# Optimization experiments

Measured on AMD Instinct MI355X. Metric: run time of the kernel, lower is better.

## Reference

```python
import jax, jax.numpy as jnp
import numpy as np

N_NODES = 50000
N_EDGES = 800000
FEAT = 128
HID = 64
N_CLS = 12


def setup_inputs() -> dict:
    key = jax.random.key(0)
    ks = jax.random.split(key, 8)
    x = jax.random.normal(ks[0], (N_NODES, FEAT), dtype=jnp.float32)
    edge_index = jax.random.randint(ks[1], (2, N_EDGES), 0, N_NODES, dtype=jnp.int64)
    s1 = 1.0 / np.sqrt(FEAT)
    s2 = 1.0 / np.sqrt(HID)
    W1 = jax.random.uniform(ks[2], (FEAT, HID), jnp.float32, -s1, s1)
    b1 = jnp.zeros((HID,), jnp.float32)
    W2 = jax.random.uniform(ks[3], (HID, HID), jnp.float32, -s2, s2)
    b2 = jnp.zeros((HID,), jnp.float32)
    Wfc = jax.random.uniform(ks[4], (HID, N_CLS), jnp.float32, -s2, s2)
    bfc = jax.random.uniform(ks[5], (N_CLS,), jnp.float32, -s2, s2)
    return {"x": x, "edge_index": edge_index, "W1": W1, "b1": b1,
            "W2": W2, "b2": b2, "Wfc": Wfc, "bfc": bfc}


def gcn_conv(x, W, b, src, dst, n_nodes):
    """PyG GCNConv: symmetric-normalized aggregation with self-loops.
    out_i = sum_{j in N(i)} (xW)_j / sqrt(d_i d_j) + (xW)_i / d_i + b,
    where d = in-degree + 1 (self loop)."""
    xw = x @ W  # [N, out] -- transform before propagate (PyG order)
    deg = jnp.zeros((n_nodes,), x.dtype).at[dst].add(1.0) + 1.0
    dinv = jax.lax.rsqrt(deg)
    norm = dinv[src] * dinv[dst]  # [E]
    agg = jax.ops.segment_sum(xw[src] * norm[:, None], dst, num_segments=n_nodes)
    agg = agg + xw * (dinv * dinv)[:, None]  # self-loop term
    return agg + b


def reference(x, edge_index, W1, b1, W2, b2, Wfc, bfc):
    n = x.shape[0]
    src, dst = edge_index[0], edge_index[1]
    h = jax.nn.relu(gcn_conv(x, W1, b1, src, dst, n))
    h = jax.nn.relu(gcn_conv(h, W2, b2, src, dst, n))
    return h @ Wfc + bfc  # [N, num_content_categories]
```

## Files before the change

### kernel.cpp

```cpp
#include <hip/hip_runtime.h>
#include <hip/hip_fp16.h>


#define CAP   64
#define NBUK  196
#define ET    2048
#define NB    391

typedef unsigned short u16;

__global__ __launch_bounds__(256) void k_hist(const int* __restrict__ dst,
                                              int* __restrict__ blkcnt, int E) {
    __shared__ int hist[NBUK];
    const int tid = threadIdx.x, blk = blockIdx.x;
    for (int i = tid; i < NBUK; i += 256) hist[i] = 0;
    __syncthreads();
    const int e0 = blk * ET;
#pragma unroll
    for (int j = 0; j < ET / 256; j++) {
        int e = e0 + j * 256 + tid;
        if (e < E) atomicAdd(&hist[(unsigned)dst[e] >> 8], 1);
    }
    __syncthreads();
    for (int b = tid; b < NBUK; b += 256) blkcnt[b * NB + blk] = hist[b];
}

__global__ __launch_bounds__(512) void k_scanA(int* __restrict__ blkcnt,
                                               int* __restrict__ btot) {
    __shared__ int s[512];
    const int t = threadIdx.x, b = blockIdx.x;
    int v = (t < NB) ? blkcnt[b * NB + t] : 0;
    s[t] = v;
    __syncthreads();
#pragma unroll
    for (int d = 1; d < 512; d <<= 1) {
        int u = (t >= d) ? s[t - d] : 0;
        __syncthreads();
        s[t] += u;
        __syncthreads();
    }
    if (t < NB) blkcnt[b * NB + t] = s[t] - v;
    if (t == 511) btot[b] = s[511];
}

__global__ __launch_bounds__(256) void k_scanB(const int* __restrict__ btot,
                                               int* __restrict__ bbase, int E) {
    __shared__ int s[256];
    const int t = threadIdx.x;
    int v = (t < NBUK) ? btot[t] : 0;
    s[t] = v;
    __syncthreads();
#pragma unroll
    for (int d = 1; d < 256; d <<= 1) {
        int u = (t >= d) ? s[t - d] : 0;
        __syncthreads();
        s[t] += u;
        __syncthreads();
    }
    if (t < NBUK) bbase[t] = s[t] - v;
    if (t == 0) bbase[NBUK] = E;
}

__global__ __launch_bounds__(256) void k_scatter(const int* __restrict__ src,
                                                 const int* __restrict__ dst,
                                                 const int* __restrict__ blkcnt,
                                                 const int* __restrict__ bbase,
                                                 unsigned* __restrict__ eb, int E) {
    __shared__ int cur[NBUK];
    const int tid = threadIdx.x, blk = blockIdx.x;
    for (int i = tid; i < NBUK; i += 256) cur[i] = blkcnt[i * NB + blk] + bbase[i];
    __syncthreads();
    const int e0 = blk * ET;
#pragma unroll
    for (int j = 0; j < ET / 256; j++) {
        int e = e0 + j * 256 + tid;
        if (e < E) {
            unsigned d = (unsigned)dst[e];
            unsigned u = (d << 16) | (unsigned)src[e];
            int p = atomicAdd(&cur[d >> 8], 1);
            eb[p] = u;
        }
    }
}

__global__ __launch_bounds__(1024) void k_buildb(const unsigned* __restrict__ eb,
                                                 const int* __restrict__ bbase,
                                                 u16* __restrict__ csr,
                                                 int* __restrict__ cnt, int n) {
    __shared__ u16 lcsr[256 * CAP];
    __shared__ int cur[256];
    const int tid = threadIdx.x, b = blockIdx.x;
    if (tid < 256) cur[tid] = 0;
    __syncthreads();
    const int e0 = bbase[b], e1 = bbase[b + 1];
    for (int e = e0 + tid; e < e1; e += 1024) {
        unsigned u = eb[e];
        int ld = (int)((u >> 16) & 255u);
        int p = atomicAdd(&cur[ld], 1);
        if (p < CAP) lcsr[ld * CAP + p] = (u16)(u & 0xffffu);
    }
    __syncthreads();
    const int node0 = b * 256;
    for (int i = tid; i < 256 * CAP / 8; i += 1024) {
        int r = i / (CAP / 8), q = i % (CAP / 8);
        int c = cur[r] < CAP ? cur[r] : CAP;
        uint4 v = *(uint4*)&lcsr[r * CAP + q * 8];
        if (q * 8 >= c) v = make_uint4(0, 0, 0, 0);
        *(uint4*)&csr[(size_t)(node0 + r) * CAP + q * 8] = v;
    }
    if (tid < 256 && node0 + tid < n) cnt[node0 + tid] = cur[tid];
}

template <int K, bool IS_HALF, typename TIN>
__global__ __launch_bounds__(256) void k_gemm(const TIN* __restrict__ X,
                                              const float* __restrict__ W,
                                              const int* __restrict__ cnt,
                                              __half* __restrict__ Y, int n) {
    constexpr int KC = 64;
    constexpr int XS = KC + 4;
    __shared__ float ws[KC * 64];
    __shared__ float xs[64 * XS];
    const int tid = threadIdx.x;
    const int tx = tid & 15;
    const int ty = tid >> 4;
    const int row0 = blockIdx.x * 64;

    float acc[4][4];
#pragma unroll
    for (int r = 0; r < 4; r++)
#pragma unroll
        for (int c = 0; c < 4; c++) acc[r][c] = 0.f;

#pragma unroll 1
    for (int kc = 0; kc < K; kc += KC) {
        for (int i = tid; i < KC * 16; i += 256) {
            int kk = i >> 4, c4 = i & 15;
            *(float4*)&ws[kk * 64 + 4 * c4] = *(const float4*)&W[(kc + kk) * 64 + 4 * c4];
        }
        if (IS_HALF) {
            for (int i = tid; i < 64 * (KC / 8); i += 256) {
                int r = i >> 3, q = i & 7;
                uint4 u = make_uint4(0, 0, 0, 0);
                int row = row0 + r;
                if (row < n) u = *(const uint4*)&X[(size_t)row * K + kc + 8 * q];
                float2 f0 = __half22float2(*(__half2*)&u.x);
                float2 f1 = __half22float2(*(__half2*)&u.y);
                float2 f2 = __half22float2(*(__half2*)&u.z);
                float2 f3 = __half22float2(*(__half2*)&u.w);
                *(float4*)&xs[r * XS + 8 * q]     = make_float4(f0.x, f0.y, f1.x, f1.y);
                *(float4*)&xs[r * XS + 8 * q + 4] = make_float4(f2.x, f2.y, f3.x, f3.y);
            }
        } else {
            for (int i = tid; i < 64 * (KC / 4); i += 256) {
                int r = i / (KC / 4), q = i % (KC / 4);
                float4 v = make_float4(0.f, 0.f, 0.f, 0.f);
                int row = row0 + r;
                if (row < n) v = *(const float4*)&((const float*)X)[(size_t)row * K + kc + 4 * q];
                *(float4*)&xs[r * XS + 4 * q] = v;
            }
        }
        __syncthreads();

#pragma unroll 2
        for (int q = 0; q < KC / 4; q++) {
            float4 xv[4];
#pragma unroll
            for (int r = 0; r < 4; r++)
                xv[r] = *(const float4*)&xs[(ty + 16 * r) * XS + 4 * q];
#pragma unroll
            for (int kk = 0; kk < 4; kk++) {
                float4 wv = *(const float4*)&ws[(4 * q + kk) * 64 + 4 * tx];
#pragma unroll
                for (int r = 0; r < 4; r++) {
                    float xval = (kk == 0) ? xv[r].x : (kk == 1) ? xv[r].y
                               : (kk == 2) ? xv[r].z : xv[r].w;
                    acc[r][0] = fmaf(xval, wv.x, acc[r][0]);
                    acc[r][1] = fmaf(xval, wv.y, acc[r][1]);
                    acc[r][2] = fmaf(xval, wv.z, acc[r][2]);
                    acc[r][3] = fmaf(xval, wv.w, acc[r][3]);
                }
            }
        }
        __syncthreads();
    }

#pragma unroll
    for (int r = 0; r < 4; r++) {
        int row = row0 + ty + 16 * r;
        if (row < n) {
            float d = rsqrtf((float)cnt[row] + 1.0f);
            __half2* yh = (__half2*)&Y[(size_t)row * 64 + 4 * tx];
            yh[0] = __floats2half2_rn(acc[r][0] * d, acc[r][1] * d);
            yh[1] = __floats2half2_rn(acc[r][2] * d, acc[r][3] * d);
        }
    }
}

__device__ __forceinline__ float2 gather_node(const __half* __restrict__ y,
                                              const u16* __restrict__ lst,
                                              int deg, int c2) {
    float2 acc = make_float2(0.f, 0.f);
    int i = 0;
    for (; i + 16 <= deg; i += 16) {
        uint4 qa = *(const uint4*)(lst + i);
        uint4 qb = *(const uint4*)(lst + i + 8);
        unsigned idx[16] = {qa.x & 0xffffu, qa.x >> 16, qa.y & 0xffffu, qa.y >> 16,
                            qa.z & 0xffffu, qa.z >> 16, qa.w & 0xffffu, qa.w >> 16,
                            qb.x & 0xffffu, qb.x >> 16, qb.y & 0xffffu, qb.y >> 16,
                            qb.z & 0xffffu, qb.z >> 16, qb.w & 0xffffu, qb.w >> 16};
        __half2 v[16];
#pragma unroll
        for (int t = 0; t < 16; t++) v[t] = *(const __half2*)&y[idx[t] * 64 + 2 * c2];
        float2 f[16];
#pragma unroll
        for (int t = 0; t < 16; t++) f[t] = __half22float2(v[t]);
#pragma unroll
        for (int s = 1; s < 16; s <<= 1)
#pragma unroll
            for (int t = 0; t < 16; t += 2 * s) { f[t].x += f[t + s].x; f[t].y += f[t + s].y; }
        acc.x += f[0].x; acc.y += f[0].y;
    }
    if (i + 8 <= deg) {
        uint4 qa = *(const uint4*)(lst + i);
        unsigned idx[8] = {qa.x & 0xffffu, qa.x >> 16, qa.y & 0xffffu, qa.y >> 16,
                           qa.z & 0xffffu, qa.z >> 16, qa.w & 0xffffu, qa.w >> 16};
        __half2 v[8];
#pragma unroll
        for (int t = 0; t < 8; t++) v[t] = *(const __half2*)&y[idx[t] * 64 + 2 * c2];
        float2 f[8];
#pragma unroll
        for (int t = 0; t < 8; t++) f[t] = __half22float2(v[t]);
#pragma unroll
        for (int s = 1; s < 8; s <<= 1)
#pragma unroll
            for (int t = 0; t < 8; t += 2 * s) { f[t].x += f[t + s].x; f[t].y += f[t + s].y; }
        acc.x += f[0].x; acc.y += f[0].y;
        i += 8;
    }
    if (i + 4 <= deg) {
        uint2 qa = *(const uint2*)(lst + i);
        unsigned idx[4] = {qa.x & 0xffffu, qa.x >> 16, qa.y & 0xffffu, qa.y >> 16};
        __half2 v[4];
#pragma unroll
        for (int t = 0; t < 4; t++) v[t] = *(const __half2*)&y[idx[t] * 64 + 2 * c2];
        float2 f0 = __half22float2(v[0]), f1 = __half22float2(v[1]);
        float2 f2 = __half22float2(v[2]), f3 = __half22float2(v[3]);
        acc.x += (f0.x + f1.x) + (f2.x + f3.x);
        acc.y += (f0.y + f1.y) + (f2.y + f3.y);
        i += 4;
    }
    for (; i < deg; i++) {
        float2 f = __half22float2(*(const __half2*)&y[lst[i] * 64 + 2 * c2]);
        acc.x += f.x; acc.y += f.y;
    }
    return acc;
}

__global__ __launch_bounds__(256) void k_agg1(const __half* __restrict__ y,
                                              const u16* __restrict__ csr,
                                              const int* __restrict__ cnt,
                                              const float* __restrict__ bias,
                                              __half* __restrict__ h1, int n) {
    const int tid = threadIdx.x;
    const int c2 = tid & 31;
    const int node = blockIdx.x * 8 + (tid >> 5);
    if (node >= n) return;
    int deg_raw = cnt[node];
    int deg = deg_raw > CAP ? CAP : deg_raw;
    float2 acc = gather_node(y, csr + node * CAP, deg, c2);
    float2 sf = __half22float2(*(const __half2*)&y[node * 64 + 2 * c2]);
    float d = rsqrtf((float)deg_raw + 1.0f);
    float2 bv = *(const float2*)&bias[2 * c2];
    float vx = fmaxf(fmaf(d, acc.x + sf.x, bv.x), 0.f);
    float vy = fmaxf(fmaf(d, acc.y + sf.y, bv.y), 0.f);
    *(__half2*)&h1[node * 64 + 2 * c2] = __floats2half2_rn(vx, vy);
}

__global__ __launch_bounds__(256) void k_agg2fc(const __half* __restrict__ y,
                                                const u16* __restrict__ csr,
                                                const int* __restrict__ cnt,
                                                const float* __restrict__ bias,
                                                const float* __restrict__ Wfc,
                                                const float* __restrict__ bfc,
                                                float* __restrict__ out, int n) {
    __shared__ float wf[12 * 64];
    __shared__ float bf[12];
    const int tid = threadIdx.x;
    for (int i = tid; i < 12 * 64; i += 256) {
        int c = i >> 6, k = i & 63;
        wf[i] = Wfc[k * 12 + c];
    }
    if (tid < 12) bf[tid] = bfc[tid];
    __syncthreads();

    const int c2 = tid & 31;
    const int node = blockIdx.x * 8 + (tid >> 5);
    if (node >= n) return;
    int deg_raw = cnt[node];
    int deg = deg_raw > CAP ? CAP : deg_raw;
    float2 acc = gather_node(y, csr + node * CAP, deg, c2);
    float2 sf = __half22float2(*(const __half2*)&y[node * 64 + 2 * c2]);
    float d = rsqrtf((float)deg_raw + 1.0f);
    float2 bv = *(const float2*)&bias[2 * c2];
    float vx = fmaxf(fmaf(d, acc.x + sf.x, bv.x), 0.f);
    float vy = fmaxf(fmaf(d, acc.y + sf.y, bv.y), 0.f);

    float res = 0.f;
#pragma unroll
    for (int c = 0; c < 12; c++) {
        float2 wv = *(const float2*)&wf[c * 64 + 2 * c2];
        float p = vx * wv.x + vy * wv.y;
        p += __shfl_xor(p, 1);
        p += __shfl_xor(p, 2);
        p += __shfl_xor(p, 4);
        p += __shfl_xor(p, 8);
        p += __shfl_xor(p, 16);
        if (c2 == c) res = p + bf[c];
    }
    if (c2 < 12) out[(size_t)node * 12 + c2] = res;
}

extern "C" void kernel_launch(void* const* d_in, const int* in_sizes, int n_in,
                              void* d_out, int out_size, void* d_ws, size_t ws_size,
                              hipStream_t stream) {
    const float* x   = (const float*)d_in[0];
    const int*   ei  = (const int*)d_in[1];
    const float* W1  = (const float*)d_in[2];
    const float* b1  = (const float*)d_in[3];
    const float* W2  = (const float*)d_in[4];
    const float* b2  = (const float*)d_in[5];
    const float* Wfc = (const float*)d_in[6];
    const float* bfc = (const float*)d_in[7];
    float* out = (float*)d_out;

    const int n = in_sizes[0] / 128;
    const int E = in_sizes[1] / 2;
    const int* src = ei;
    const int* dst = ei + E;

    char* w = (char*)d_ws;
    unsigned* eb  = (unsigned*)w;  w += (size_t)((E + 63) / 64) * 64 * 4;
    int* blkcnt   = (int*)w;       w += (size_t)NBUK * NB * 4 + 256;
    int* btot     = (int*)w;       w += 256 * 4;
    int* bbase    = (int*)w;       w += (NBUK + 64) * 4;
    int* cnt      = (int*)w;       w += (size_t)((n + 63) / 64) * 64 * 4;
    u16* csr      = (u16*)w;       w += (size_t)NBUK * 256 * CAP * 2;
    __half* y     = (__half*)w;    w += (size_t)n * 64 * 2;
    __half* h1    = (__half*)w;

    k_hist   <<<dim3(NB), dim3(256), 0, stream>>>(dst, blkcnt, E);
    k_scanA  <<<dim3(NBUK), dim3(512), 0, stream>>>(blkcnt, btot);
    k_scanB  <<<dim3(1), dim3(256), 0, stream>>>(btot, bbase, E);
    k_scatter<<<dim3(NB), dim3(256), 0, stream>>>(src, dst, blkcnt, bbase, eb, E);
    k_buildb <<<dim3(NBUK), dim3(1024), 0, stream>>>(eb, bbase, csr, cnt, n);
    k_gemm<128, false, float><<<dim3((n + 63) / 64), dim3(256), 0, stream>>>(x, W1, cnt, y, n);
    k_agg1   <<<dim3((n + 7) / 8), dim3(256), 0, stream>>>(y, csr, cnt, b1, h1, n);
    k_gemm<64, true, __half><<<dim3((n + 63) / 64), dim3(256), 0, stream>>>(h1, W2, cnt, y, n);
    k_agg2fc <<<dim3((n + 7) / 8), dim3(256), 0, stream>>>(y, csr, cnt, b2, Wfc, bfc, out, n);
}
```

Baseline: 189.6 us.

## Vectorize edge loads, fold bucket scan into consumers, widen gather to 4 channels

Doubles edges per block in the histogram and scatter kernels and loads src/dst as int4 vectors. The separate single-block bucket scan kernel is removed; each scatter and buildb block recomputes the 196-entry prefix in shared memory instead. The aggregation kernels now have 16 lanes per node, each gathering 4 half channels per neighbor with uint2 loads, which halves the load instruction count and shortens the FC shuffle reduction. The trade-offs are redundant per-block scan work and fewer blocks for the preprocessing stages.

```diff
diff --git a/kernel.cpp b/kernel.cpp
--- a/kernel.cpp
+++ b/kernel.cpp
@@ -4,8 +4,8 @@
 
 #define CAP   64
 #define NBUK  196
-#define ET    2048
-#define NB    391
+#define ET    4096
+#define NB    196
 
 typedef unsigned short u16;
 
@@ -16,83 +16,112 @@
     for (int i = tid; i < NBUK; i += 256) hist[i] = 0;
     __syncthreads();
     const int e0 = blk * ET;
-#pragma unroll
-    for (int j = 0; j < ET / 256; j++) {
-        int e = e0 + j * 256 + tid;
-        if (e < E) atomicAdd(&hist[(unsigned)dst[e] >> 8], 1);
+    if (e0 + ET <= E) {
+        const int4* d4 = (const int4*)(dst + e0);
+#pragma unroll
+        for (int j = 0; j < ET / 1024; j++) {
+            int4 d = d4[j * 256 + tid];
+            atomicAdd(&hist[(unsigned)d.x >> 8], 1);
+            atomicAdd(&hist[(unsigned)d.y >> 8], 1);
+            atomicAdd(&hist[(unsigned)d.z >> 8], 1);
+            atomicAdd(&hist[(unsigned)d.w >> 8], 1);
+        }
+    } else {
+        for (int j = 0; j < ET / 256; j++) {
+            int e = e0 + j * 256 + tid;
+            if (e < E) atomicAdd(&hist[(unsigned)dst[e] >> 8], 1);
+        }
     }
     __syncthreads();
     for (int b = tid; b < NBUK; b += 256) blkcnt[b * NB + blk] = hist[b];
 }
 
-__global__ __launch_bounds__(512) void k_scanA(int* __restrict__ blkcnt,
+__global__ __launch_bounds__(256) void k_scanA(int* __restrict__ blkcnt,
                                                int* __restrict__ btot) {
-    __shared__ int s[512];
+    __shared__ int s[256];
     const int t = threadIdx.x, b = blockIdx.x;
     int v = (t < NB) ? blkcnt[b * NB + t] : 0;
     s[t] = v;
     __syncthreads();
 #pragma unroll
-    for (int d = 1; d < 512; d <<= 1) {
-        int u = (t >= d) ? s[t - d] : 0;
-        __syncthreads();
-        s[t] += u;
-        __syncthreads();
-    }
-    if (t < NB) blkcnt[b * NB + t] = s[t] - v;
-    if (t == 511) btot[b] = s[511];
-}
-
-__global__ __launch_bounds__(256) void k_scanB(const int* __restrict__ btot,
-                                               int* __restrict__ bbase, int E) {
-    __shared__ int s[256];
-    const int t = threadIdx.x;
-    int v = (t < NBUK) ? btot[t] : 0;
-    s[t] = v;
-    __syncthreads();
-#pragma unroll
     for (int d = 1; d < 256; d <<= 1) {
         int u = (t >= d) ? s[t - d] : 0;
         __syncthreads();
         s[t] += u;
         __syncthreads();
     }
-    if (t < NBUK) bbase[t] = s[t] - v;
-    if (t == 0) bbase[NBUK] = E;
+    if (t < NB) blkcnt[b * NB + t] = s[t] - v;
+    if (t == 255) btot[b] = s[255];
+}
+
+__device__ __forceinline__ void local_bucket_scan(const int* __restrict__ btot,
+                                                  int* bb, int tid) {
+    if (tid < 256) bb[tid] = (tid < NBUK) ? btot[tid] : 0;
+    __syncthreads();
+#pragma unroll
+    for (int d = 1; d < 256; d <<= 1) {
+        int u = 0;
+        if (tid < 256 && tid >= d) u = bb[tid - d];
+        __syncthreads();
+        if (tid < 256) bb[tid] += u;
+        __syncthreads();
+    }
+    if (tid < 256) bb[tid] -= (tid < NBUK) ? btot[tid] : 0;
+    __syncthreads();
 }
 
 __global__ __launch_bounds__(256) void k_scatter(const int* __restrict__ src,
                                                  const int* __restrict__ dst,
                                                  const int* __restrict__ blkcnt,
-                                                 const int* __restrict__ bbase,
+                                                 const int* __restrict__ btot,
                                                  unsigned* __restrict__ eb, int E) {
+    __shared__ int bb[256];
     __shared__ int cur[NBUK];
     const int tid = threadIdx.x, blk = blockIdx.x;
-    for (int i = tid; i < NBUK; i += 256) cur[i] = blkcnt[i * NB + blk] + bbase[i];
+    local_bucket_scan(btot, bb, tid);
+    for (int i = tid; i < NBUK; i += 256) cur[i] = blkcnt[i * NB + blk] + bb[i];
     __syncthreads();
     const int e0 = blk * ET;
-#pragma unroll
-    for (int j = 0; j < ET / 256; j++) {
-        int e = e0 + j * 256 + tid;
-        if (e < E) {
-            unsigned d = (unsigned)dst[e];
-            unsigned u = (d << 16) | (unsigned)src[e];
-            int p = atomicAdd(&cur[d >> 8], 1);
-            eb[p] = u;
+    if (e0 + ET <= E) {
+        const int4* s4 = (const int4*)(src + e0);
+        const int4* d4 = (const int4*)(dst + e0);
+#pragma unroll
+        for (int j = 0; j < ET / 1024; j++) {
+            int4 sv = s4[j * 256 + tid];
+            int4 dv = d4[j * 256 + tid];
+            unsigned u0 = ((unsigned)dv.x << 16) | (unsigned)sv.x;
+            unsigned u1 = ((unsigned)dv.y << 16) | (unsigned)sv.y;
+            unsigned u2 = ((unsigned)dv.z << 16) | (unsigned)sv.z;
+            unsigned u3 = ((unsigned)dv.w << 16) | (unsigned)sv.w;
+            eb[atomicAdd(&cur[u0 >> 24], 1)] = u0;
+            eb[atomicAdd(&cur[u1 >> 24], 1)] = u1;
+            eb[atomicAdd(&cur[u2 >> 24], 1)] = u2;
+            eb[atomicAdd(&cur[u3 >> 24], 1)] = u3;
+        }
+    } else {
+        for (int j = 0; j < ET / 256; j++) {
+            int e = e0 + j * 256 + tid;
+            if (e < E) {
+                unsigned d = (unsigned)dst[e];
+                unsigned u = (d << 16) | (unsigned)src[e];
+                eb[atomicAdd(&cur[d >> 8], 1)] = u;
+            }
         }
     }
 }
 
 __global__ __launch_bounds__(1024) void k_buildb(const unsigned* __restrict__ eb,
-                                                 const int* __restrict__ bbase,
+                                                 const int* __restrict__ btot,
                                                  u16* __restrict__ csr,
                                                  int* __restrict__ cnt, int n) {
+    __shared__ int bb[256];
     __shared__ u16 lcsr[256 * CAP];
     __shared__ int cur[256];
     const int tid = threadIdx.x, b = blockIdx.x;
+    local_bucket_scan(btot, bb, tid);
     if (tid < 256) cur[tid] = 0;
     __syncthreads();
-    const int e0 = bbase[b], e1 = bbase[b + 1];
+    const int e0 = bb[b], e1 = bb[b] + btot[b];
     for (int e = e0 + tid; e < e1; e += 1024) {
         unsigned u = eb[e];
         int ld = (int)((u >> 16) & 255u);
@@ -196,10 +225,11 @@
     }
 }
 
-__device__ __forceinline__ float2 gather_node(const __half* __restrict__ y,
+__device__ __forceinline__ float4 gather_node(const __half* __restrict__ y,
                                               const u16* __restrict__ lst,
-                                              int deg, int c2) {
-    float2 acc = make_float2(0.f, 0.f);
+                                              int deg, int c4) {
+    float4 a0 = make_float4(0.f, 0.f, 0.f, 0.f);
+    float4 a1 = make_float4(0.f, 0.f, 0.f, 0.f);
     int i = 0;
     for (; i + 16 <= deg; i += 16) {
         uint4 qa = *(const uint4*)(lst + i);
@@ -208,52 +238,61 @@
                             qa.z & 0xffffu, qa.z >> 16, qa.w & 0xffffu, qa.w >> 16,
                             qb.x & 0xffffu, qb.x >> 16, qb.y & 0xffffu, qb.y >> 16,
                             qb.z & 0xffffu, qb.z >> 16, qb.w & 0xffffu, qb.w >> 16};
-        __half2 v[16];
-#pragma unroll
-        for (int t = 0; t < 16; t++) v[t] = *(const __half2*)&y[idx[t] * 64 + 2 * c2];
-        float2 f[16];
-#pragma unroll
-        for (int t = 0; t < 16; t++) f[t] = __half22float2(v[t]);
-#pragma unroll
-        for (int s = 1; s < 16; s <<= 1)
-#pragma unroll
-            for (int t = 0; t < 16; t += 2 * s) { f[t].x += f[t + s].x; f[t].y += f[t + s].y; }
-        acc.x += f[0].x; acc.y += f[0].y;
+        uint2 v[16];
+#pragma unroll
+        for (int t = 0; t < 16; t++) v[t] = *(const uint2*)&y[idx[t] * 64 + 4 * c4];
+#pragma unroll
+        for (int t = 0; t < 16; t += 2) {
+            float2 lo0 = __half22float2(*(__half2*)&v[t].x);
+            float2 hi0 = __half22float2(*(__half2*)&v[t].y);
+            float2 lo1 = __half22float2(*(__half2*)&v[t + 1].x);
+            float2 hi1 = __half22float2(*(__half2*)&v[t + 1].y);
+            a0.x += lo0.x; a0.y += lo0.y; a0.z += hi0.x; a0.w += hi0.y;
+            a1.x += lo1.x; a1.y += lo1.y; a1.z += hi1.x; a1.w += hi1.y;
+        }
     }
     if (i + 8 <= deg) {
         uint4 qa = *(const uint4*)(lst + i);
         unsigned idx[8] = {qa.x & 0xffffu, qa.x >> 16, qa.y & 0xffffu, qa.y >> 16,
                            qa.z & 0xffffu, qa.z >> 16, qa.w & 0xffffu, qa.w >> 16};
-        __half2 v[8];
-#pragma unroll
-        for (int t = 0; t < 8; t++) v[t] = *(const __half2*)&y[idx[t] * 64 + 2 * c2];
-        float2 f[8];
-#pragma unroll
-        for (int t = 0; t < 8; t++) f[t] = __half22float2(v[t]);
-#pragma unroll
-        for (int s = 1; s < 8; s <<= 1)
-#pragma unroll
-            for (int t = 0; t < 8; t += 2 * s) { f[t].x += f[t + s].x; f[t].y += f[t + s].y; }
-        acc.x += f[0].x; acc.y += f[0].y;
+        uint2 v[8];
+#pragma unroll
+        for (int t = 0; t < 8; t++) v[t] = *(const uint2*)&y[idx[t] * 64 + 4 * c4];
+#pragma unroll
+        for (int t = 0; t < 8; t += 2) {
+            float2 lo0 = __half22float2(*(__half2*)&v[t].x);
+            float2 hi0 = __half22float2(*(__half2*)&v[t].y);
+            float2 lo1 = __half22float2(*(__half2*)&v[t + 1].x);
+            float2 hi1 = __half22float2(*(__half2*)&v[t + 1].y);
+            a0.x += lo0.x; a0.y += lo0.y; a0.z += hi0.x; a0.w += hi0.y;
+            a1.x += lo1.x; a1.y += lo1.y; a1.z += hi1.x; a1.w += hi1.y;
+        }
         i += 8;
     }
     if (i + 4 <= deg) {
         uint2 qa = *(const uint2*)(lst + i);
         unsigned idx[4] = {qa.x & 0xffffu, qa.x >> 16, qa.y & 0xffffu, qa.y >> 16};
-        __half2 v[4];
-#pragma unroll
-        for (int t = 0; t < 4; t++) v[t] = *(const __half2*)&y[idx[t] * 64 + 2 * c2];
-        float2 f0 = __half22float2(v[0]), f1 = __half22float2(v[1]);
-        float2 f2 = __half22float2(v[2]), f3 = __half22float2(v[3]);
-        acc.x += (f0.x + f1.x) + (f2.x + f3.x);
-        acc.y += (f0.y + f1.y) + (f2.y + f3.y);
+        uint2 v[4];
+#pragma unroll
+        for (int t = 0; t < 4; t++) v[t] = *(const uint2*)&y[idx[t] * 64 + 4 * c4];
+#pragma unroll
+        for (int t = 0; t < 4; t += 2) {
+            float2 lo0 = __half22float2(*(__half2*)&v[t].x);
+            float2 hi0 = __half22float2(*(__half2*)&v[t].y);
+            float2 lo1 = __half22float2(*(__half2*)&v[t + 1].x);
+            float2 hi1 = __half22float2(*(__half2*)&v[t + 1].y);
+            a0.x += lo0.x; a0.y += lo0.y; a0.z += hi0.x; a0.w += hi0.y;
+            a1.x += lo1.x; a1.y += lo1.y; a1.z += hi1.x; a1.w += hi1.y;
+        }
         i += 4;
     }
     for (; i < deg; i++) {
-        float2 f = __half22float2(*(const __half2*)&y[lst[i] * 64 + 2 * c2]);
-        acc.x += f.x; acc.y += f.y;
-    }
-    return acc;
+        uint2 vv = *(const uint2*)&y[lst[i] * 64 + 4 * c4];
+        float2 lo = __half22float2(*(__half2*)&vv.x);
+        float2 hi = __half22float2(*(__half2*)&vv.y);
+        a0.x += lo.x; a0.y += lo.y; a0.z += hi.x; a0.w += hi.y;
+    }
+    return make_float4(a0.x + a1.x, a0.y + a1.y, a0.z + a1.z, a0.w + a1.w);
 }
 
 __global__ __launch_bounds__(256) void k_agg1(const __half* __restrict__ y,
@@ -262,18 +301,25 @@
                                               const float* __restrict__ bias,
                                               __half* __restrict__ h1, int n) {
     const int tid = threadIdx.x;
-    const int c2 = tid & 31;
-    const int node = blockIdx.x * 8 + (tid >> 5);
+    const int c4 = tid & 15;
+    const int node = blockIdx.x * 16 + (tid >> 4);
     if (node >= n) return;
     int deg_raw = cnt[node];
     int deg = deg_raw > CAP ? CAP : deg_raw;
-    float2 acc = gather_node(y, csr + node * CAP, deg, c2);
-    float2 sf = __half22float2(*(const __half2*)&y[node * 64 + 2 * c2]);
+    float4 acc = gather_node(y, csr + node * CAP, deg, c4);
+    uint2 sv = *(const uint2*)&y[node * 64 + 4 * c4];
+    float2 slo = __half22float2(*(__half2*)&sv.x);
+    float2 shi = __half22float2(*(__half2*)&sv.y);
     float d = rsqrtf((float)deg_raw + 1.0f);
-    float2 bv = *(const float2*)&bias[2 * c2];
-    float vx = fmaxf(fmaf(d, acc.x + sf.x, bv.x), 0.f);
-    float vy = fmaxf(fmaf(d, acc.y + sf.y, bv.y), 0.f);
-    *(__half2*)&h1[node * 64 + 2 * c2] = __floats2half2_rn(vx, vy);
+    float4 bv = *(const float4*)&bias[4 * c4];
+    float v0 = fmaxf(fmaf(d, acc.x + slo.x, bv.x), 0.f);
+    float v1 = fmaxf(fmaf(d, acc.y + slo.y, bv.y), 0.f);
+    float v2 = fmaxf(fmaf(d, acc.z + shi.x, bv.z), 0.f);
+    float v3 = fmaxf(fmaf(d, acc.w + shi.y, bv.w), 0.f);
+    uint2 o;
+    *(__half2*)&o.x = __floats2half2_rn(v0, v1);
+    *(__half2*)&o.y = __floats2half2_rn(v2, v3);
+    *(uint2*)&h1[node * 64 + 4 * c4] = o;
 }
 
 __global__ __launch_bounds__(256) void k_agg2fc(const __half* __restrict__ y,
@@ -293,31 +339,34 @@
     if (tid < 12) bf[tid] = bfc[tid];
     __syncthreads();
 
-    const int c2 = tid & 31;
-    const int node = blockIdx.x * 8 + (tid >> 5);
+    const int c4 = tid & 15;
+    const int node = blockIdx.x * 16 + (tid >> 4);
     if (node >= n) return;
     int deg_raw = cnt[node];
     int deg = deg_raw > CAP ? CAP : deg_raw;
-    float2 acc = gather_node(y, csr + node * CAP, deg, c2);
-    float2 sf = __half22float2(*(const __half2*)&y[node * 64 + 2 * c2]);
+    float4 acc = gather_node(y, csr + node * CAP, deg, c4);
+    uint2 sv = *(const uint2*)&y[node * 64 + 4 * c4];
+    float2 slo = __half22float2(*(__half2*)&sv.x);
+    float2 shi = __half22float2(*(__half2*)&sv.y);
     float d = rsqrtf((float)deg_raw + 1.0f);
-    float2 bv = *(const float2*)&bias[2 * c2];
-    float vx = fmaxf(fmaf(d, acc.x + sf.x, bv.x), 0.f);
-    float vy = fmaxf(fmaf(d, acc.y + sf.y, bv.y), 0.f);
+    float4 bv = *(const float4*)&bias[4 * c4];
+    float v0 = fmaxf(fmaf(d, acc.x + slo.x, bv.x), 0.f);
+    float v1 = fmaxf(fmaf(d, acc.y + slo.y, bv.y), 0.f);
+    float v2 = fmaxf(fmaf(d, acc.z + shi.x, bv.z), 0.f);
+    float v3 = fmaxf(fmaf(d, acc.w + shi.y, bv.w), 0.f);
 
     float res = 0.f;
 #pragma unroll
     for (int c = 0; c < 12; c++) {
-        float2 wv = *(const float2*)&wf[c * 64 + 2 * c2];
-        float p = vx * wv.x + vy * wv.y;
+        float4 wv = *(const float4*)&wf[c * 64 + 4 * c4];
+        float p = v0 * wv.x + v1 * wv.y + v2 * wv.z + v3 * wv.w;
         p += __shfl_xor(p, 1);
         p += __shfl_xor(p, 2);
         p += __shfl_xor(p, 4);
         p += __shfl_xor(p, 8);
-        p += __shfl_xor(p, 16);
-        if (c2 == c) res = p + bf[c];
-    }
-    if (c2 < 12) out[(size_t)node * 12 + c2] = res;
+        if (c4 == c) res = p + bf[c];
+    }
+    if (c4 < 12) out[(size_t)node * 12 + c4] = res;
 }
 
 extern "C" void kernel_launch(void* const* d_in, const int* in_sizes, int n_in,
@@ -337,24 +386,23 @@
     const int E = in_sizes[1] / 2;
     const int* src = ei;
     const int* dst = ei + E;
+    const int nblk = (E + ET - 1) / ET;
 
     char* w = (char*)d_ws;
     unsigned* eb  = (unsigned*)w;  w += (size_t)((E + 63) / 64) * 64 * 4;
     int* blkcnt   = (int*)w;       w += (size_t)NBUK * NB * 4 + 256;
     int* btot     = (int*)w;       w += 256 * 4;
-    int* bbase    = (int*)w;       w += (NBUK + 64) * 4;
     int* cnt      = (int*)w;       w += (size_t)((n + 63) / 64) * 64 * 4;
     u16* csr      = (u16*)w;       w += (size_t)NBUK * 256 * CAP * 2;
     __half* y     = (__half*)w;    w += (size_t)n * 64 * 2;
     __half* h1    = (__half*)w;
 
-    k_hist   <<<dim3(NB), dim3(256), 0, stream>>>(dst, blkcnt, E);
-    k_scanA  <<<dim3(NBUK), dim3(512), 0, stream>>>(blkcnt, btot);
-    k_scanB  <<<dim3(1), dim3(256), 0, stream>>>(btot, bbase, E);
-    k_scatter<<<dim3(NB), dim3(256), 0, stream>>>(src, dst, blkcnt, bbase, eb, E);
-    k_buildb <<<dim3(NBUK), dim3(1024), 0, stream>>>(eb, bbase, csr, cnt, n);
+    k_hist   <<<dim3(nblk), dim3(256), 0, stream>>>(dst, blkcnt, E);
+    k_scanA  <<<dim3(NBUK), dim3(256), 0, stream>>>(blkcnt, btot);
+    k_scatter<<<dim3(nblk), dim3(256), 0, stream>>>(src, dst, blkcnt, btot, eb, E);
+    k_buildb <<<dim3(NBUK), dim3(1024), 0, stream>>>(eb, btot, csr, cnt, n);
     k_gemm<128, false, float><<<dim3((n + 63) / 64), dim3(256), 0, stream>>>(x, W1, cnt, y, n);
-    k_agg1   <<<dim3((n + 7) / 8), dim3(256), 0, stream>>>(y, csr, cnt, b1, h1, n);
+    k_agg1   <<<dim3((n + 15) / 16), dim3(256), 0, stream>>>(y, csr, cnt, b1, h1, n);
     k_gemm<64, true, __half><<<dim3((n + 63) / 64), dim3(256), 0, stream>>>(h1, W2, cnt, y, n);
-    k_agg2fc <<<dim3((n + 7) / 8), dim3(256), 0, stream>>>(y, csr, cnt, b2, Wfc, bfc, out, n);
-}
+    k_agg2fc <<<dim3((n + 15) / 16), dim3(256), 0, stream>>>(y, csr, cnt, b2, Wfc, bfc, out, n);
+}
```

After: 186.9 us. Within noise of the previous version (-1.4%).
